# Optimization experiments

Measured on AMD Instinct MI355X. Metric: run time of the kernel, lower is better.

Reference implementation:

```python
import jax, jax.numpy as jnp
import numpy as np

B, S, D = 16, 512, 512
H, HS, HSEL = 8, 2, 2      # heads, shared heads, selected routed heads
NB = 2                     # num_block -> L = 3*NB layers (NB knowledge + 2*NB question)
L = 3 * NB
DFF = 2048


def setup_inputs() -> dict:
    key = jax.random.key(0)
    ks = jax.random.split(key, 12)
    s = 0.02
    return {
        'question_emb': jax.random.normal(ks[0], (B, S, D), jnp.float32),
        'interaction_emb': jax.random.normal(ks[1], (B, S, D), jnp.float32),
        'wq': jax.random.normal(ks[2], (L, D, D), jnp.float32) * s,
        'bq': jnp.zeros((L, D), jnp.float32),
        'wv': jax.random.normal(ks[3], (L, D, D), jnp.float32) * s,
        'bv': jnp.zeros((L, D), jnp.float32),
        'wo': jax.random.normal(ks[4], (L, D, D), jnp.float32) * s,
        'bo': jnp.zeros((L, D), jnp.float32),
        'wg': jax.random.normal(ks[5], (L, D, H - HS), jnp.float32) * s,
        'ln1_g': jnp.ones((L, D), jnp.float32),
        'ln1_b': jnp.zeros((L, D), jnp.float32),
        'fw1': jax.random.normal(ks[6], (L, D, DFF), jnp.float32) * s,
        'fb1': jnp.zeros((L, DFF), jnp.float32),
        'fw2': jax.random.normal(ks[7], (L, DFF, D), jnp.float32) * s,
        'fb2': jnp.zeros((L, D), jnp.float32),
        'ln2_g': jnp.ones((L, D), jnp.float32),
        'ln2_b': jnp.zeros((L, D), jnp.float32),
    }


def _ln(x, g, b, eps=1e-5):
    mu = x.mean(-1, keepdims=True)
    var = ((x - mu) ** 2).mean(-1, keepdims=True)
    return g * (x - mu) / jnp.sqrt(var + eps) + b


def _forward(question_emb, interaction_emb, wq, bq, wv, bv, wo, bo, wg,
             ln1_g, ln1_b, fw1, fb1, fw2, fb2, ln2_g, ln2_b):
    def block(x_q, x_v, i, mask_flag, apply_pos):
        b, s, d = x_q.shape
        dk = d // H
        # mask_flag=True -> allow j<=i (strict future masked); False -> allow j<i
        allowed = jnp.tril(jnp.ones((s, s), bool), 0 if mask_flag else -1)
        qlin = x_q @ wq[i] + bq[i]                                   # kq_same: k = q
        v = (x_v @ wv[i] + bv[i]).reshape(b, s, H, dk).transpose(0, 2, 1, 3)
        qh = qlin.reshape(b, s, H, dk).transpose(0, 2, 1, 3)         # [b,h,s,dk]
        scores = jnp.einsum('bhqd,bhkd->bhqk', qh, qh) / jnp.sqrt(jnp.float32(dk))
        scores = jnp.where(allowed[None, None], scores, jnp.float32(-1e9))
        scores = scores.at[:, :, 0, :].set(0.0)                      # pad_zero row 0
        # dynamic head routing over non-shared heads
        gates = jax.nn.softmax((qlin @ wg[i]).reshape(b * s, H - HS), axis=-1)
        _, idx = jax.lax.top_k(gates, HSEL)
        dmask = jnp.zeros_like(gates).at[jnp.arange(b * s)[:, None], idx].set(1.0)
        dyn = (gates * dmask).reshape(b, s, H - HS)
        rmask = jnp.concatenate([jnp.ones((b, s, HS), gates.dtype), dyn], axis=-1)
        rmask = rmask.mean(axis=1)                                   # [b,H]
        attn = jax.nn.softmax(scores, axis=-1)
        ctx = jnp.einsum('bhqk,bhkd->bhqd', attn, v) * rmask[:, :, None, None]
        ctx = ctx.transpose(0, 2, 1, 3).reshape(b, s, d)
        x = _ln(x_q + ctx @ wo[i] + bo[i], ln1_g[i], ln1_b[i])
        if apply_pos:
            ffn = jax.nn.relu(x @ fw1[i] + fb1[i]) @ fw2[i] + fb2[i]
            x = _ln(x + ffn, ln2_g[i], ln2_b[i])
        return x

    y = interaction_emb
    for i in range(NB):                 # knowledge encoder
        y = block(y, y, i, True, False)
    x = question_emb
    li = NB
    for j in range(2 * NB):             # question encoder, alternating
        if j % 2 == 0:
            x = block(x, x, li, True, False)
        else:
            x = block(x, y, li, False, True)
        li += 1
    return x


def reference(question_emb, interaction_emb, wq, bq, wv, bv, wo, bo, wg,
              ln1_g, ln1_b, fw1, fb1, fw2, fb2, ln2_g, ln2_b):
    return _forward(question_emb, interaction_emb, wq, bq, wv, bv, wo, bo, wg,
                    ln1_g, ln1_b, fw1, fb1, fw2, fb2, ln2_g, ln2_b)
```

## Files before the change

### kernel.cpp

```cpp
#include <hip/hip_runtime.h>
#include <hip/hip_bf16.h>

#define BSZ 16
#define SEQ 512
#define DIM 512
#define NH 8
#define DK 64
#define NROWS (BSZ*SEQ)
#define DFF2 2048

typedef unsigned short u16;
typedef u16   u16x8 __attribute__((ext_vector_type(8)));
typedef short s16x8 __attribute__((ext_vector_type(8)));
typedef float f32x4 __attribute__((ext_vector_type(4)));

__device__ __forceinline__ u16 f2b(float x) {
    union { float f; unsigned int u; } c; c.f = x;
    unsigned int r = c.u + 0x7fff + ((c.u >> 16) & 1);
    return (u16)(r >> 16);
}
__device__ __forceinline__ float b2f(u16 u) {
    union { unsigned int i; float f; } c; c.i = ((unsigned int)u) << 16; return c.f;
}

__device__ __forceinline__ void gld16(const u16* g, u16* l) {
    __builtin_amdgcn_global_load_lds(
        (const __attribute__((address_space(1))) unsigned int*)(unsigned long long)g,
        (__attribute__((address_space(3))) unsigned int*)(unsigned int)(unsigned long long)l,
        16, 0, 0);
}

__global__ __launch_bounds__(256) void cast_f2b4(const float* __restrict__ in,
                                                 u16* __restrict__ out, int n4) {
    int i = blockIdx.x * 256 + threadIdx.x;
    if (i >= n4) return;
    float4 v = ((const float4*)in)[i];
    ushort4 o; o.x = f2b(v.x); o.y = f2b(v.y); o.z = f2b(v.z); o.w = f2b(v.w);
    ((ushort4*)out)[i] = o;
}

__global__ __launch_bounds__(256) void transpose_cast(
    const float* __restrict__ W, u16* __restrict__ WT,
    int K, int N, int layer0, int lstride, size_t dstride)
{
    __shared__ float t[32][33];
    int z = blockIdx.z;
    const float* Wz = W + (size_t)(layer0 + z * lstride) * K * N;
    u16* WTz = WT + (size_t)z * dstride;
    int k0 = blockIdx.x * 32, n0 = blockIdx.y * 32;
    int tx = threadIdx.x & 31, ty = threadIdx.x >> 5;
    for (int i = ty; i < 32; i += 8) t[i][tx] = Wz[(size_t)(k0 + i) * N + n0 + tx];
    __syncthreads();
    for (int i = ty; i < 32; i += 8) WTz[(size_t)(n0 + i) * K + k0 + tx] = f2b(t[tx][i]);
}

template<int WRITE_BF16, int RELU, int SPLIT, int SPLITK, int NI>
__global__ __launch_bounds__(256) void gemm2(
    const u16* __restrict__ Aq, const u16* __restrict__ Av,
    const u16* __restrict__ WT,
    const float* __restrict__ bias1, const float* __restrict__ bias2,
    void* __restrict__ C1, void* __restrict__ C2,
    int K, int lda, int ldw, int ldc, int nsplit, int nx)
{
    __shared__ __attribute__((aligned(16))) u16 As[2][128 * 32];
    __shared__ __attribute__((aligned(16))) u16 Bs[2][NI * 32 * 32];
    int tid = threadIdx.x;
    int wave = tid >> 6, lane = tid & 63;
    int quad = lane >> 4, l16 = lane & 15;

    int bid = blockIdx.x;
    int per = gridDim.x >> 3;
    int swz = (bid & 7) * per + (bid >> 3);
    int nxy = SPLITK ? ((int)gridDim.x >> 1) : (int)gridDim.x;
    int kslice = 0;
    if (SPLITK && swz >= nxy) { kslice = 1; swz -= nxy; }
    int bx = swz % nx, by = swz / nx;
    int n0 = bx * (NI * 32), m0 = by * 128;

    int wrow = (wave & 1) * 64;
    int wcol = (wave >> 1) * (NI * 16);
    bool isv = SPLIT && (n0 >= nsplit);
    const u16* A = isv ? Av : Aq;

    int sr = wave * 32 + (lane >> 2);
    int sc = (lane & 3) * 8;
    int ko = kslice * K;
    const u16* gA0 = A  + (size_t)(m0 + sr) * lda + sc + ko;
    const u16* gA1 = gA0 + (size_t)16 * lda;
    int lo0 = (wave * 32) * 32;
    int lo1 = (wave * 32 + 16) * 32;

    const u16* gB0;
    const u16* gB1 = nullptr;
    int bo0, bo1 = 0;
    if (NI == 4) {
        gB0 = WT + (size_t)(n0 + sr) * ldw + sc + ko;
        gB1 = gB0 + (size_t)16 * ldw;
        bo0 = lo0; bo1 = lo1;
    } else {
        gB0 = WT + (size_t)(n0 + wave * 16 + (lane >> 2)) * ldw + sc + ko;
        bo0 = (wave * 16) * 32;
    }

    f32x4 acc[4][NI];
    #pragma unroll
    for (int i = 0; i < 4; i++)
        #pragma unroll
        for (int j = 0; j < NI; j++) acc[i][j] = (f32x4){0.f, 0.f, 0.f, 0.f};

    gld16(gA0, &As[0][lo0]);
    gld16(gA1, &As[0][lo1]);
    gld16(gB0, &Bs[0][bo0]);
    if (NI == 4) gld16(gB1, &Bs[0][bo1]);
    __syncthreads();

    int NT = K >> 5;
    int cur = 0;
    for (int t = 0; t < NT; ++t) {
        if (t + 1 < NT) {
            int k0 = (t + 1) << 5;
            gld16(gA0 + k0, &As[cur ^ 1][lo0]);
            gld16(gA1 + k0, &As[cur ^ 1][lo1]);
            gld16(gB0 + k0, &Bs[cur ^ 1][bo0]);
            if (NI == 4) gld16(gB1 + k0, &Bs[cur ^ 1][bo1]);
        }
        s16x8 af[4], bf[NI];
        #pragma unroll
        for (int i = 0; i < 4; i++)
            af[i] = *(s16x8*)&As[cur][(wrow + i * 16 + l16) * 32 + quad * 8];
        #pragma unroll
        for (int i = 0; i < NI; i++)
            bf[i] = *(s16x8*)&Bs[cur][(wcol + i * 16 + l16) * 32 + quad * 8];
        #pragma unroll
        for (int mi = 0; mi < 4; mi++)
            #pragma unroll
            for (int ni = 0; ni < NI; ni++)
                acc[mi][ni] = __builtin_amdgcn_mfma_f32_16x16x32_bf16(
                    af[mi], bf[ni], acc[mi][ni], 0, 0, 0);
        __syncthreads();
        cur ^= 1;
    }

    const float* bias = isv ? bias2 : bias1;
    void* C = (isv || (SPLITK && kslice)) ? C2 : C1;
    int nb = n0 - (isv ? nsplit : 0);
    #pragma unroll
    for (int ni = 0; ni < NI; ni++) {
        int cn = nb + wcol + ni * 16 + l16;
        float bb = bias ? bias[cn] : 0.f;
        #pragma unroll
        for (int mi = 0; mi < 4; mi++) {
            int cm = m0 + wrow + mi * 16 + quad * 4;
            #pragma unroll
            for (int r = 0; r < 4; r++) {
                size_t off = (size_t)(cm + r) * ldc + cn;
                float v = acc[mi][ni][r] + bb;
                if (RELU) v = fmaxf(v, 0.f);
                if (WRITE_BF16) ((u16*)C)[off] = f2b(v);
                else            ((float*)C)[off] = v;
            }
        }
    }
}

__global__ void init_rmask6(float* __restrict__ r) {
    int t = blockIdx.x * 256 + threadIdx.x;
    if (t < 6 * 128) r[t] = ((t & 7) < 2) ? 1.0f : 0.0f;
}

__global__ __launch_bounds__(256) void router_kernel(
    const u16* __restrict__ qlin, const float* __restrict__ wg,
    float* __restrict__ rmask)
{
    __shared__ float s_wg[6 * 544];
    __shared__ float sacc[8];
    int tid = threadIdx.x;
    #pragma unroll
    for (int k = 0; k < 12; k++) {
        int n = tid + k * 256;
        int d = n / 6, r = n - d * 6;
        s_wg[r * 544 + (d >> 4) * 17 + (d & 15)] = wg[n];
    }
    if (tid < 8) sacc[tid] = 0.f;
    __syncthreads();

    int c = tid & 31;
    int row = blockIdx.x * 8 + (tid >> 5);
    int cb = c * 17;
    const u16* xr = qlin + (size_t)row * DIM + c * 16;
    u16x8 q0 = *(const u16x8*)xr;
    u16x8 q1 = *(const u16x8*)(xr + 8);

    float lg[6] = {0.f, 0.f, 0.f, 0.f, 0.f, 0.f};
    #pragma unroll
    for (int j = 0; j < 8; j++) {
        float x = b2f(q0[j]);
        #pragma unroll
        for (int r = 0; r < 6; r++) lg[r] += x * s_wg[r * 544 + cb + j];
    }
    #pragma unroll
    for (int j = 0; j < 8; j++) {
        float x = b2f(q1[j]);
        #pragma unroll
        for (int r = 0; r < 6; r++) lg[r] += x * s_wg[r * 544 + cb + 8 + j];
    }
    #pragma unroll
    for (int r = 0; r < 6; r++) {
        #pragma unroll
        for (int o = 1; o < 32; o <<= 1) lg[r] += __shfl_xor(lg[r], o);
    }
    float m = lg[0];
    #pragma unroll
    for (int r = 1; r < 6; r++) m = fmaxf(m, lg[r]);
    float s = 0.f;
    #pragma unroll
    for (int r = 0; r < 6; r++) { lg[r] = __expf(lg[r] - m); s += lg[r]; }
    float inv = 1.0f / s;
    #pragma unroll
    for (int r = 0; r < 6; r++) lg[r] *= inv;
    int i1 = 0; float g1 = lg[0];
    #pragma unroll
    for (int r = 1; r < 6; r++) if (lg[r] > g1) { g1 = lg[r]; i1 = r; }
    int i2 = -1; float g2 = -1.f;
    #pragma unroll
    for (int r = 0; r < 6; r++) if (r != i1 && lg[r] > g2) { g2 = lg[r]; i2 = r; }
    if (c == 0) {
        atomicAdd(&sacc[i1], g1);
        atomicAdd(&sacc[i2], g2);
    }
    __syncthreads();
    if (tid < 6) {
        int b = blockIdx.x >> 6;
        atomicAdd(&rmask[b * 8 + 2 + tid], sacc[tid] * (1.0f / (float)SEQ));
    }
}

__global__ __launch_bounds__(256) void transpose_v(
    const u16* __restrict__ v, u16* __restrict__ vT)
{
    __shared__ u16 t[64][72];
    int jt = blockIdx.x, bh = blockIdx.y;
    int b = bh >> 3, h = bh & 7;
    int tid = threadIdx.x;
    int lr = tid >> 2, lc = (tid & 3) * 16;
    const u16* src = v + (size_t)(b * SEQ + jt * 64 + lr) * DIM + h * DK + lc;
    *(u16x8*)&t[lr][lc]     = *(const u16x8*)src;
    *(u16x8*)&t[lr][lc + 8] = *(const u16x8*)(src + 8);
    __syncthreads();
    u16x8 o0, o1;
    #pragma unroll
    for (int i = 0; i < 8; i++) o0[i] = t[lc + i][lr];
    #pragma unroll
    for (int i = 0; i < 8; i++) o1[i] = t[lc + 8 + i][lr];
    u16* dst = vT + ((size_t)bh * DK + lr) * SEQ + jt * 64 + lc;
    *(u16x8*)dst       = o0;
    *(u16x8*)(dst + 8) = o1;
}

__global__ __launch_bounds__(256) void attn_flash(
    const u16* __restrict__ qlin, const u16* __restrict__ vT,
    const float* __restrict__ rmask, u16* __restrict__ ctx, int mask_flag)
{
    __shared__ u16 s_q [64][72];
    __shared__ u16 s_k [64][72];
    __shared__ u16 s_vt[64][72];
    __shared__ u16 s_p [64][72];
    int qt = blockIdx.x, h = blockIdx.y, b = blockIdx.z;
    int tid = threadIdx.x;
    int wave = tid >> 6, lane = tid & 63;
    int quad = lane >> 4, l16 = lane & 15;
    int lr = tid >> 2, lc = (tid & 3) * 16;

    {
        const u16* src = qlin + (size_t)(b * SEQ + qt * 64 + lr) * DIM + h * DK + lc;
        *(u16x8*)&s_q[lr][lc]     = *(const u16x8*)src;
        *(u16x8*)&s_q[lr][lc + 8] = *(const u16x8*)(src + 8);
    }

    f32x4 acc_o[4];
    #pragma unroll
    for (int i = 0; i < 4; i++) acc_o[i] = (f32x4){0.f, 0.f, 0.f, 0.f};
    float m_i[4] = {-1e30f, -1e30f, -1e30f, -1e30f};
    float l_i[4] = {0.f, 0.f, 0.f, 0.f};

    for (int jt = 0; jt <= qt; jt++) {
        const u16* ksrc = qlin + (size_t)(b * SEQ + jt * 64 + lr) * DIM + h * DK + lc;
        const u16* vtsrc = vT + ((size_t)(b * NH + h) * DK + lr) * SEQ + jt * 64 + lc;
        u16x8 k0 = *(const u16x8*)ksrc,  k1 = *(const u16x8*)(ksrc + 8);
        u16x8 v0 = *(const u16x8*)vtsrc, v1 = *(const u16x8*)(vtsrc + 8);
        __syncthreads();
        *(u16x8*)&s_k[lr][lc]      = k0;
        *(u16x8*)&s_k[lr][lc + 8]  = k1;
        *(u16x8*)&s_vt[lr][lc]     = v0;
        *(u16x8*)&s_vt[lr][lc + 8] = v1;
        __syncthreads();

        f32x4 acc_s[4];
        #pragma unroll
        for (int i = 0; i < 4; i++) acc_s[i] = (f32x4){0.f, 0.f, 0.f, 0.f};
        #pragma unroll
        for (int ks = 0; ks < 2; ks++) {
            s16x8 a = *(s16x8*)&s_q[wave * 16 + l16][ks * 32 + quad * 8];
            #pragma unroll
            for (int nf = 0; nf < 4; nf++) {
                s16x8 bb = *(s16x8*)&s_k[nf * 16 + l16][ks * 32 + quad * 8];
                acc_s[nf] = __builtin_amdgcn_mfma_f32_16x16x32_bf16(a, bb, acc_s[nf], 0, 0, 0);
            }
        }

        int qg0 = qt * 64 + wave * 16 + quad * 4;
        float sc[4][4];
        #pragma unroll
        for (int nf = 0; nf < 4; nf++) {
            int jg = jt * 64 + nf * 16 + l16;
            #pragma unroll
            for (int r = 0; r < 4; r++) {
                float v = acc_s[nf][r] * 0.125f;
                if (jt == qt) {
                    int bound = mask_flag ? (qg0 + r) : (qg0 + r - 1);
                    if (jg > bound) v = -1e30f;
                }
                sc[nf][r] = v;
            }
        }
        float tmax[4];
        #pragma unroll
        for (int r = 0; r < 4; r++) {
            float t = fmaxf(fmaxf(sc[0][r], sc[1][r]), fmaxf(sc[2][r], sc[3][r]));
            #pragma unroll
            for (int o = 1; o < 16; o <<= 1) t = fmaxf(t, __shfl_xor(t, o));
            tmax[r] = t;
        }
        float p[4][4];
        #pragma unroll
        for (int r = 0; r < 4; r++) {
            float mnew = fmaxf(m_i[r], tmax[r]);
            float alpha = __expf(m_i[r] - mnew);
            float su = 0.f;
            #pragma unroll
            for (int nf = 0; nf < 4; nf++) { p[nf][r] = __expf(sc[nf][r] - mnew); su += p[nf][r]; }
            #pragma unroll
            for (int o = 1; o < 16; o <<= 1) su += __shfl_xor(su, o);
            l_i[r] = l_i[r] * alpha + su;
            m_i[r] = mnew;
            #pragma unroll
            for (int nf = 0; nf < 4; nf++) acc_o[nf][r] *= alpha;
        }
        #pragma unroll
        for (int nf = 0; nf < 4; nf++)
            #pragma unroll
            for (int r = 0; r < 4; r++)
                s_p[wave * 16 + quad * 4 + r][nf * 16 + l16] = f2b(p[nf][r]);

        #pragma unroll
        for (int ks = 0; ks < 2; ks++) {
            s16x8 a = *(s16x8*)&s_p[wave * 16 + l16][ks * 32 + quad * 8];
            #pragma unroll
            for (int nf = 0; nf < 4; nf++) {
                s16x8 bb = *(s16x8*)&s_vt[nf * 16 + l16][ks * 32 + quad * 8];
                acc_o[nf] = __builtin_amdgcn_mfma_f32_16x16x32_bf16(a, bb, acc_o[nf], 0, 0, 0);
            }
        }
    }

    float rm = rmask[b * 8 + h];
    int qrow = qt * 64 + wave * 16 + quad * 4;
    #pragma unroll
    for (int r = 0; r < 4; r++) {
        float scale = rm / l_i[r];
        u16* dst = ctx + (size_t)(b * SEQ + qrow + r) * DIM + h * DK;
        #pragma unroll
        for (int nf = 0; nf < 4; nf++)
            dst[nf * 16 + l16] = f2b(acc_o[nf][r] * scale);
    }
}

__global__ __launch_bounds__(256) void attn_row0(
    const u16* __restrict__ vT, const float* __restrict__ rmask, u16* __restrict__ ctx)
{
    int bh = blockIdx.x;
    int b = bh >> 3, h = bh & 7;
    int d = threadIdx.x >> 2, seg = threadIdx.x & 3;
    const u16* src = vT + ((size_t)bh * DK + d) * SEQ + seg * 128;
    float s = 0.f;
    for (int i = 0; i < 16; i++) {
        u16x8 v = *(const u16x8*)(src + i * 8);
        #pragma unroll
        for (int j = 0; j < 8; j++) s += b2f(v[j]);
    }
    s += __shfl_down(s, 1);
    s += __shfl_down(s, 2);
    if (seg == 0)
        ctx[(size_t)(b * SEQ) * DIM + h * DK + d] =
            f2b(s * (1.0f / (float)SEQ) * rmask[b * 8 + h]);
}

__global__ __launch_bounds__(256) void add_ln2(
    float* __restrict__ x, const float* __restrict__ p0, const float* __restrict__ p1,
    const float* __restrict__ bcol,
    const float* __restrict__ g, const float* __restrict__ bta,
    u16* __restrict__ out16)
{
    __shared__ float redA[4], redB[4];
    int row = blockIdx.x, tid = threadIdx.x;
    size_t base = (size_t)row * DIM;
    float t0 = x[base + tid]       + p0[base + tid]       + p1[base + tid]       + bcol[tid];
    float t1 = x[base + tid + 256] + p0[base + tid + 256] + p1[base + tid + 256] + bcol[tid + 256];
    float s = t0 + t1, sq = t0 * t0 + t1 * t1;
    for (int o = 32; o > 0; o >>= 1) { s += __shfl_down(s, o, 64); sq += __shfl_down(sq, o, 64); }
    int lane = tid & 63, wid = tid >> 6;
    if (lane == 0) { redA[wid] = s; redB[wid] = sq; }
    __syncthreads();
    float S1 = redA[0] + redA[1] + redA[2] + redA[3];
    float S2 = redB[0] + redB[1] + redB[2] + redB[3];
    float mu = S1 * (1.0f / (float)DIM);
    float var = S2 * (1.0f / (float)DIM) - mu * mu;
    float rstd = rsqrtf(var + 1e-5f);
    float o0 = g[tid]       * (t0 - mu) * rstd + bta[tid];
    float o1 = g[tid + 256] * (t1 - mu) * rstd + bta[tid + 256];
    x[base + tid]       = o0;
    x[base + tid + 256] = o1;
    out16[base + tid]       = f2b(o0);
    out16[base + tid + 256] = f2b(o1);
}

extern "C" void kernel_launch(void* const* d_in, const int* in_sizes, int n_in,
                              void* d_out, int out_size, void* d_ws, size_t ws_size,
                              hipStream_t stream) {
    const float* qe   = (const float*)d_in[0];
    const float* ie   = (const float*)d_in[1];
    const float* wq   = (const float*)d_in[2];
    const float* bq   = (const float*)d_in[3];
    const float* wv   = (const float*)d_in[4];
    const float* bv   = (const float*)d_in[5];
    const float* wo   = (const float*)d_in[6];
    const float* bo   = (const float*)d_in[7];
    const float* wg   = (const float*)d_in[8];
    const float* ln1g = (const float*)d_in[9];
    const float* ln1b = (const float*)d_in[10];
    const float* fw1  = (const float*)d_in[11];
    const float* fb1  = (const float*)d_in[12];
    const float* fw2  = (const float*)d_in[13];
    const float* fb2  = (const float*)d_in[14];
    const float* ln2g = (const float*)d_in[15];
    const float* ln2b = (const float*)d_in[16];

    const size_t RD = (size_t)NROWS * DIM;
    float* ws   = (float*)d_ws;
    float* xbuf = ws;
    float* ybuf = ws + RD;

    u16* b16    = (u16*)(ws + 2 * RD);
    u16* x16    = b16;                 b16 += RD;
    u16* y16    = b16;                 b16 += RD;
    u16* ctx16  = b16;                 b16 += RD;
    u16* qlin16 = b16;                 b16 += RD;
    u16* vbuf16 = b16;                 b16 += RD;
    u16* vT     = b16;                 b16 += RD;
    float* proj0 = (float*)vbuf16;
    u16* hid    = b16;                 b16 += 4 * RD;
    float* proj1 = (float*)b16;        b16 += 2 * RD;
    u16* wqvT   = b16;                 b16 += 6 * (size_t)1024 * 512;
    u16* woT    = b16;                 b16 += 6 * (size_t)512 * 512;
    u16* fw1T   = b16;                 b16 += 2 * (size_t)DFF2 * 512;
    u16* fw2T   = b16;                 b16 += 2 * (size_t)512 * DFF2;
    float* rmask6 = (float*)b16;

    const size_t nBytes = RD * sizeof(float);
    hipMemcpyAsync(xbuf, qe, nBytes, hipMemcpyDeviceToDevice, stream);
    hipMemcpyAsync(ybuf, ie, nBytes, hipMemcpyDeviceToDevice, stream);
    cast_f2b4<<<(int)(RD / 4 / 256), 256, 0, stream>>>(qe, x16, (int)(RD / 4));
    cast_f2b4<<<(int)(RD / 4 / 256), 256, 0, stream>>>(ie, y16, (int)(RD / 4));

    transpose_cast<<<dim3(16, 16, 6), 256, 0, stream>>>(wq, wqvT,             512, 512, 0, 1, (size_t)1024 * 512);
    transpose_cast<<<dim3(16, 16, 6), 256, 0, stream>>>(wv, wqvT + 512 * 512, 512, 512, 0, 1, (size_t)1024 * 512);
    transpose_cast<<<dim3(16, 16, 6), 256, 0, stream>>>(wo, woT,              512, 512, 0, 1, (size_t)512 * 512);
    transpose_cast<<<dim3(16, 64, 2), 256, 0, stream>>>(fw1, fw1T, 512, DFF2, 3, 2, (size_t)DFF2 * 512);
    transpose_cast<<<dim3(64, 16, 2), 256, 0, stream>>>(fw2, fw2T, DFF2, 512, 3, 2, (size_t)512 * DFF2);
    init_rmask6<<<3, 256, 0, stream>>>(rmask6);

    const int BIG = 1 << 30;
    auto run_block = [&](float* xr, u16* xq16, const u16* xv16, int l, int maskf, int pos) {
        size_t lD = (size_t)l * DIM;
        float* rm = rmask6 + l * 128;
        gemm2<1, 0, 1, 0, 2><<<1024, 256, 0, stream>>>(
            xq16, xv16, wqvT + (size_t)l * 1024 * 512, bq + lD, bv + lD,
            qlin16, vbuf16, 512, 512, 512, 512, 512, 16);
        transpose_v<<<dim3(8, 128), 256, 0, stream>>>(vbuf16, vT);
        router_kernel<<<NROWS / 8, 256, 0, stream>>>(qlin16, wg + (size_t)l * DIM * 6, rm);
        attn_flash<<<dim3(SEQ / 64, NH, BSZ), 256, 0, stream>>>(qlin16, vT, rm, ctx16, maskf);
        attn_row0<<<128, 256, 0, stream>>>(vT, rm, ctx16);
        gemm2<0, 0, 0, 1, 2><<<1024, 256, 0, stream>>>(
            ctx16, ctx16, woT + (size_t)l * 512 * 512, nullptr, nullptr,
            proj0, proj1, 256, 512, 512, 512, BIG, 8);
        add_ln2<<<NROWS, 256, 0, stream>>>(xr, proj0, proj1, bo + lD,
                                           ln1g + lD, ln1b + lD, xq16);
        if (pos) {
            int slot = (l - 3) / 2;
            gemm2<1, 1, 0, 0, 2><<<2048, 256, 0, stream>>>(
                xq16, xq16, fw1T + (size_t)slot * DFF2 * 512,
                fb1 + (size_t)l * DFF2, nullptr,
                hid, nullptr, 512, 512, 512, DFF2, BIG, 32);
            gemm2<0, 0, 0, 1, 2><<<1024, 256, 0, stream>>>(
                hid, hid, fw2T + (size_t)slot * 512 * DFF2, nullptr, nullptr,
                proj0, proj1, 1024, DFF2, DFF2, 512, BIG, 8);
            add_ln2<<<NROWS, 256, 0, stream>>>(xr, proj0, proj1, fb2 + lD,
                                               ln2g + lD, ln2b + lD, xq16);
        }
    };

    run_block(ybuf, y16, y16, 0, 1, 0);
    run_block(ybuf, y16, y16, 1, 1, 0);
    run_block(xbuf, x16, x16, 2, 1, 0);
    run_block(xbuf, x16, y16, 3, 0, 1);
    run_block(xbuf, x16, x16, 4, 1, 0);
    run_block(xbuf, x16, y16, 5, 0, 1);

    hipMemcpyAsync(d_out, xbuf, nBytes, hipMemcpyDeviceToDevice, stream);
}
```

Baseline: 925.4 us.

## Load attention K/V fragments directly from global memory and remap grid for XCD locality

The flash attention kernel stops staging Q, K and V^T tiles in shared memory and instead loads the MFMA operand fragments straight from global memory into registers. This removes the two block-wide barriers per key tile, leaving only per-wave barriers around the P tile in LDS. The launch becomes a 1D grid whose block index is swizzled so blocks for the same batch and head are grouped, likely per XCD. The trade-off is redundant global/L2 reads, since each of the four waves loads the full K and V tiles, and the fragment loads are less coalesced.

```diff
diff --git a/kernel.cpp b/kernel.cpp
--- a/kernel.cpp
+++ b/kernel.cpp
@@ -261,21 +261,21 @@
     const u16* __restrict__ qlin, const u16* __restrict__ vT,
     const float* __restrict__ rmask, u16* __restrict__ ctx, int mask_flag)
 {
-    __shared__ u16 s_q [64][72];
-    __shared__ u16 s_k [64][72];
-    __shared__ u16 s_vt[64][72];
-    __shared__ u16 s_p [64][72];
-    int qt = blockIdx.x, h = blockIdx.y, b = blockIdx.z;
+    __shared__ u16 s_p[64][72];
+    int gi = (blockIdx.x & 7) * ((int)gridDim.x >> 3) + (blockIdx.x >> 3);
+    int qt = gi & 7, h = (gi >> 3) & 7, b = gi >> 6;
     int tid = threadIdx.x;
     int wave = tid >> 6, lane = tid & 63;
     int quad = lane >> 4, l16 = lane & 15;
-    int lr = tid >> 2, lc = (tid & 3) * 16;
-
-    {
-        const u16* src = qlin + (size_t)(b * SEQ + qt * 64 + lr) * DIM + h * DK + lc;
-        *(u16x8*)&s_q[lr][lc]     = *(const u16x8*)src;
-        *(u16x8*)&s_q[lr][lc + 8] = *(const u16x8*)(src + 8);
-    }
+
+    const u16* qbase = qlin + (size_t)(b * SEQ) * DIM + h * DK;
+    const u16* vbase = vT + (size_t)(b * NH + h) * DK * SEQ;
+
+    s16x8 aq[2];
+    #pragma unroll
+    for (int ks = 0; ks < 2; ks++)
+        aq[ks] = *(const s16x8*)(qbase + (size_t)(qt * 64 + wave * 16 + l16) * DIM
+                                 + ks * 32 + quad * 8);
 
     f32x4 acc_o[4];
     #pragma unroll
@@ -284,29 +284,23 @@
     float l_i[4] = {0.f, 0.f, 0.f, 0.f};
 
     for (int jt = 0; jt <= qt; jt++) {
-        const u16* ksrc = qlin + (size_t)(b * SEQ + jt * 64 + lr) * DIM + h * DK + lc;
-        const u16* vtsrc = vT + ((size_t)(b * NH + h) * DK + lr) * SEQ + jt * 64 + lc;
-        u16x8 k0 = *(const u16x8*)ksrc,  k1 = *(const u16x8*)(ksrc + 8);
-        u16x8 v0 = *(const u16x8*)vtsrc, v1 = *(const u16x8*)(vtsrc + 8);
-        __syncthreads();
-        *(u16x8*)&s_k[lr][lc]      = k0;
-        *(u16x8*)&s_k[lr][lc + 8]  = k1;
-        *(u16x8*)&s_vt[lr][lc]     = v0;
-        *(u16x8*)&s_vt[lr][lc + 8] = v1;
-        __syncthreads();
+        s16x8 kf[2][4];
+        #pragma unroll
+        for (int ks = 0; ks < 2; ks++)
+            #pragma unroll
+            for (int nf = 0; nf < 4; nf++)
+                kf[ks][nf] = *(const s16x8*)(qbase
+                    + (size_t)(jt * 64 + nf * 16 + l16) * DIM + ks * 32 + quad * 8);
 
         f32x4 acc_s[4];
         #pragma unroll
         for (int i = 0; i < 4; i++) acc_s[i] = (f32x4){0.f, 0.f, 0.f, 0.f};
         #pragma unroll
-        for (int ks = 0; ks < 2; ks++) {
-            s16x8 a = *(s16x8*)&s_q[wave * 16 + l16][ks * 32 + quad * 8];
-            #pragma unroll
-            for (int nf = 0; nf < 4; nf++) {
-                s16x8 bb = *(s16x8*)&s_k[nf * 16 + l16][ks * 32 + quad * 8];
-                acc_s[nf] = __builtin_amdgcn_mfma_f32_16x16x32_bf16(a, bb, acc_s[nf], 0, 0, 0);
-            }
-        }
+        for (int ks = 0; ks < 2; ks++)
+            #pragma unroll
+            for (int nf = 0; nf < 4; nf++)
+                acc_s[nf] = __builtin_amdgcn_mfma_f32_16x16x32_bf16(
+                    aq[ks], kf[ks][nf], acc_s[nf], 0, 0, 0);
 
         int qg0 = qt * 64 + wave * 16 + quad * 4;
         float sc[4][4];
@@ -351,16 +345,25 @@
             #pragma unroll
             for (int r = 0; r < 4; r++)
                 s_p[wave * 16 + quad * 4 + r][nf * 16 + l16] = f2b(p[nf][r]);
-
-        #pragma unroll
-        for (int ks = 0; ks < 2; ks++) {
-            s16x8 a = *(s16x8*)&s_p[wave * 16 + l16][ks * 32 + quad * 8];
-            #pragma unroll
-            for (int nf = 0; nf < 4; nf++) {
-                s16x8 bb = *(s16x8*)&s_vt[nf * 16 + l16][ks * 32 + quad * 8];
-                acc_o[nf] = __builtin_amdgcn_mfma_f32_16x16x32_bf16(a, bb, acc_o[nf], 0, 0, 0);
-            }
-        }
+        __builtin_amdgcn_wave_barrier();
+        s16x8 pa[2];
+        pa[0] = *(s16x8*)&s_p[wave * 16 + l16][quad * 8];
+        pa[1] = *(s16x8*)&s_p[wave * 16 + l16][32 + quad * 8];
+
+        s16x8 vf[2][4];
+        #pragma unroll
+        for (int ks = 0; ks < 2; ks++)
+            #pragma unroll
+            for (int nf = 0; nf < 4; nf++)
+                vf[ks][nf] = *(const s16x8*)(vbase
+                    + (size_t)(nf * 16 + l16) * SEQ + jt * 64 + ks * 32 + quad * 8);
+        #pragma unroll
+        for (int ks = 0; ks < 2; ks++)
+            #pragma unroll
+            for (int nf = 0; nf < 4; nf++)
+                acc_o[nf] = __builtin_amdgcn_mfma_f32_16x16x32_bf16(
+                    pa[ks], vf[ks][nf], acc_o[nf], 0, 0, 0);
+        __builtin_amdgcn_wave_barrier();
     }
 
     float rm = rmask[b * 8 + h];
@@ -488,7 +491,7 @@
             qlin16, vbuf16, 512, 512, 512, 512, 512, 16);
         transpose_v<<<dim3(8, 128), 256, 0, stream>>>(vbuf16, vT);
         router_kernel<<<NROWS / 8, 256, 0, stream>>>(qlin16, wg + (size_t)l * DIM * 6, rm);
-        attn_flash<<<dim3(SEQ / 64, NH, BSZ), 256, 0, stream>>>(qlin16, vT, rm, ctx16, maskf);
+        attn_flash<<<1024, 256, 0, stream>>>(qlin16, vT, rm, ctx16, maskf);
         attn_row0<<<128, 256, 0, stream>>>(vT, rm, ctx16);
         gemm2<0, 0, 0, 1, 2><<<1024, 256, 0, stream>>>(
             ctx16, ctx16, woT + (size_t)l * 512 * 512, nullptr, nullptr,
```

Result: slower. 1.092 ms (+18.0%).

## Prefetch next K/V tile in registers, keep Q in registers, remap attention grid

Applied to the files above, without the earlier changes.

The flash attention kernel now loads the Q fragments straight into registers instead of staging them through shared memory. It prefetches the next K and V^T tiles into registers while the current tile is being computed, so global load latency overlaps with the MFMA work. The P fragments are read back once per tile, between wave barriers. The grid is flattened to 1D with a block-index permutation that interleaves causal tile lengths across workgroups to balance load across CUs. The cost is higher register pressure, and the P read-back relies on wave-level ordering for correctness.

```diff
diff --git a/kernel.cpp b/kernel.cpp
--- a/kernel.cpp
+++ b/kernel.cpp
@@ -261,21 +261,29 @@
     const u16* __restrict__ qlin, const u16* __restrict__ vT,
     const float* __restrict__ rmask, u16* __restrict__ ctx, int mask_flag)
 {
-    __shared__ u16 s_q [64][72];
     __shared__ u16 s_k [64][72];
     __shared__ u16 s_vt[64][72];
     __shared__ u16 s_p [64][72];
-    int qt = blockIdx.x, h = blockIdx.y, b = blockIdx.z;
+    int gi = (blockIdx.x & 7) * ((int)gridDim.x >> 3) + (blockIdx.x >> 3);
+    int qt = gi & 7, h = (gi >> 3) & 7, b = gi >> 6;
     int tid = threadIdx.x;
     int wave = tid >> 6, lane = tid & 63;
     int quad = lane >> 4, l16 = lane & 15;
     int lr = tid >> 2, lc = (tid & 3) * 16;
 
-    {
-        const u16* src = qlin + (size_t)(b * SEQ + qt * 64 + lr) * DIM + h * DK + lc;
-        *(u16x8*)&s_q[lr][lc]     = *(const u16x8*)src;
-        *(u16x8*)&s_q[lr][lc + 8] = *(const u16x8*)(src + 8);
-    }
+    const u16* qbase = qlin + (size_t)(b * SEQ) * DIM + h * DK;
+    const u16* vbase = vT + (size_t)(b * NH + h) * DK * SEQ;
+
+    s16x8 aq[2];
+    #pragma unroll
+    for (int ks = 0; ks < 2; ks++)
+        aq[ks] = *(const s16x8*)(qbase + (size_t)(qt * 64 + wave * 16 + l16) * DIM
+                                 + ks * 32 + quad * 8);
+
+    const u16* ks0 = qbase + (size_t)lr * DIM + lc;
+    const u16* vs0 = vbase + (size_t)lr * SEQ + lc;
+    u16x8 k0 = *(const u16x8*)ks0, k1 = *(const u16x8*)(ks0 + 8);
+    u16x8 v0 = *(const u16x8*)vs0, v1 = *(const u16x8*)(vs0 + 8);
 
     f32x4 acc_o[4];
     #pragma unroll
@@ -284,27 +292,28 @@
     float l_i[4] = {0.f, 0.f, 0.f, 0.f};
 
     for (int jt = 0; jt <= qt; jt++) {
-        const u16* ksrc = qlin + (size_t)(b * SEQ + jt * 64 + lr) * DIM + h * DK + lc;
-        const u16* vtsrc = vT + ((size_t)(b * NH + h) * DK + lr) * SEQ + jt * 64 + lc;
-        u16x8 k0 = *(const u16x8*)ksrc,  k1 = *(const u16x8*)(ksrc + 8);
-        u16x8 v0 = *(const u16x8*)vtsrc, v1 = *(const u16x8*)(vtsrc + 8);
         __syncthreads();
         *(u16x8*)&s_k[lr][lc]      = k0;
         *(u16x8*)&s_k[lr][lc + 8]  = k1;
         *(u16x8*)&s_vt[lr][lc]     = v0;
         *(u16x8*)&s_vt[lr][lc + 8] = v1;
         __syncthreads();
+        if (jt < qt) {
+            const u16* kn = qbase + (size_t)((jt + 1) * 64 + lr) * DIM + lc;
+            const u16* vn = vbase + (size_t)lr * SEQ + (jt + 1) * 64 + lc;
+            k0 = *(const u16x8*)kn;  k1 = *(const u16x8*)(kn + 8);
+            v0 = *(const u16x8*)vn;  v1 = *(const u16x8*)(vn + 8);
+        }
 
         f32x4 acc_s[4];
         #pragma unroll
         for (int i = 0; i < 4; i++) acc_s[i] = (f32x4){0.f, 0.f, 0.f, 0.f};
         #pragma unroll
         for (int ks = 0; ks < 2; ks++) {
-            s16x8 a = *(s16x8*)&s_q[wave * 16 + l16][ks * 32 + quad * 8];
             #pragma unroll
             for (int nf = 0; nf < 4; nf++) {
                 s16x8 bb = *(s16x8*)&s_k[nf * 16 + l16][ks * 32 + quad * 8];
-                acc_s[nf] = __builtin_amdgcn_mfma_f32_16x16x32_bf16(a, bb, acc_s[nf], 0, 0, 0);
+                acc_s[nf] = __builtin_amdgcn_mfma_f32_16x16x32_bf16(aq[ks], bb, acc_s[nf], 0, 0, 0);
             }
         }
 
@@ -351,14 +360,18 @@
             #pragma unroll
             for (int r = 0; r < 4; r++)
                 s_p[wave * 16 + quad * 4 + r][nf * 16 + l16] = f2b(p[nf][r]);
+        __builtin_amdgcn_wave_barrier();
+        s16x8 pa[2];
+        pa[0] = *(s16x8*)&s_p[wave * 16 + l16][quad * 8];
+        pa[1] = *(s16x8*)&s_p[wave * 16 + l16][32 + quad * 8];
+        __builtin_amdgcn_wave_barrier();
 
         #pragma unroll
         for (int ks = 0; ks < 2; ks++) {
-            s16x8 a = *(s16x8*)&s_p[wave * 16 + l16][ks * 32 + quad * 8];
             #pragma unroll
             for (int nf = 0; nf < 4; nf++) {
                 s16x8 bb = *(s16x8*)&s_vt[nf * 16 + l16][ks * 32 + quad * 8];
-                acc_o[nf] = __builtin_amdgcn_mfma_f32_16x16x32_bf16(a, bb, acc_o[nf], 0, 0, 0);
+                acc_o[nf] = __builtin_amdgcn_mfma_f32_16x16x32_bf16(pa[ks], bb, acc_o[nf], 0, 0, 0);
             }
         }
     }
@@ -488,7 +501,7 @@
             qlin16, vbuf16, 512, 512, 512, 512, 512, 16);
         transpose_v<<<dim3(8, 128), 256, 0, stream>>>(vbuf16, vT);
         router_kernel<<<NROWS / 8, 256, 0, stream>>>(qlin16, wg + (size_t)l * DIM * 6, rm);
-        attn_flash<<<dim3(SEQ / 64, NH, BSZ), 256, 0, stream>>>(qlin16, vT, rm, ctx16, maskf);
+        attn_flash<<<1024, 256, 0, stream>>>(qlin16, vT, rm, ctx16, maskf);
         attn_row0<<<128, 256, 0, stream>>>(vT, rm, ctx16);
         gemm2<0, 0, 0, 1, 2><<<1024, 256, 0, stream>>>(
             ctx16, ctx16, woT + (size_t)l * 512 * 512, nullptr, nullptr,
```

New measurement: 894.4 us. 1.03x faster.
